# Kernel optimization log

Hardware: AMD Instinct MI355X
Metric: run time of the kernel (lower is better)

The kernel has to match this reference:

```python
import jax, jax.numpy as jnp
import numpy as np

HIDDEN = 2048
HEADS = 16
HEAD_DIM = HIDDEN // HEADS
TOP_K = 256
B, N = 1, 2048


def setup_inputs() -> dict:
    key = jax.random.key(0)
    ks = jax.random.split(key, 9)
    s = 0.02
    return {
        "hidden_states": jax.random.normal(ks[0], (B, N, HIDDEN), jnp.float32),
        "Wq": jax.random.normal(ks[1], (HIDDEN, HIDDEN), jnp.float32) * s,
        "bq": jnp.zeros((HIDDEN,), jnp.float32),
        "Wk": jax.random.normal(ks[2], (HIDDEN, HIDDEN), jnp.float32) * s,
        "bk": jnp.zeros((HIDDEN,), jnp.float32),
        "Wv": jax.random.normal(ks[3], (HIDDEN, HIDDEN), jnp.float32) * s,
        "bv": jnp.zeros((HIDDEN,), jnp.float32),
        "Wo": jax.random.normal(ks[4], (HIDDEN, HIDDEN), jnp.float32) * s,
        "bo": jnp.zeros((HIDDEN,), jnp.float32),
    }


def _split_heads(x):
    b, n, _ = x.shape
    return x.reshape(b, n, HEADS, HEAD_DIM).transpose(0, 2, 1, 3)  # b h n d


def reference(hidden_states, Wq, bq, Wk, bk, Wv, bv, Wo, bo):
    scale = 1.0 / jnp.sqrt(jnp.float32(HEAD_DIM))
    q = _split_heads(hidden_states @ Wq + bq)  # [b,h,n,d]
    k = _split_heads(hidden_states @ Wk + bk)
    v = _split_heads(hidden_states @ Wv + bv)

    # Sparse path (kv_seq_length > attention_window): dense QK^T used only to rank keys.
    scores = jnp.einsum("bhnd,bhmd->bhnm", q, k) * scale  # [b,h,n,n]
    importance = scores.mean(axis=2)  # [b,h,n] aggregate over queries
    _, idx = jax.lax.top_k(importance, TOP_K)  # [b,h,k]

    # gather selected K/V (torch.gather along seq dim)
    k_sel = jnp.take_along_axis(k, idx[..., None], axis=2)  # [b,h,k,d]
    v_sel = jnp.take_along_axis(v, idx[..., None], axis=2)

    w = jax.nn.softmax(jnp.einsum("bhnd,bhkd->bhnk", q, k_sel) * scale, axis=-1)
    out = jnp.einsum("bhnk,bhkd->bhnd", w, v_sel)  # [b,h,n,d]
    out = out.transpose(0, 2, 1, 3).reshape(hidden_states.shape[0], -1, HIDDEN)
    return out @ Wo + bo
```

## Files before the change

kernel.cpp:

```cpp
#include <hip/hip_runtime.h>


typedef __attribute__((ext_vector_type(8))) short bf16x8;
typedef __attribute__((ext_vector_type(8))) unsigned short u16x8;
typedef __attribute__((ext_vector_type(4))) float f32x4;

__device__ __forceinline__ unsigned short f2bf(float x) {
    unsigned u = __float_as_uint(x);
    u += 0x7fffu + ((u >> 16) & 1u);
    return (unsigned short)(u >> 16);
}

__device__ __forceinline__ void load_lds16(const unsigned short* g, unsigned short* l) {
    __builtin_amdgcn_global_load_lds(
        (const __attribute__((address_space(1))) unsigned int*)g,
        (__attribute__((address_space(3))) unsigned int*)l,
        16, 0, 0);
}

struct Ptr4  { const float* p[4]; };

__global__ __launch_bounds__(256) void gemm_qkv(
    const unsigned short* __restrict__ HSb,
    const unsigned short* __restrict__ WT4,
    const float* __restrict__ bq,
    const float* __restrict__ bk,
    const float* __restrict__ bv,
    const int* __restrict__ idx,
    unsigned short* __restrict__ Qb,
    unsigned short* __restrict__ Ksel,
    unsigned short* __restrict__ VselT)
{
    __shared__ __align__(16) unsigned short As[4][128][32];
    __shared__ __align__(16) unsigned short Bs[4][64][32];

    const int tid  = threadIdx.x;
    const int lane = tid & 63;
    const int wave = tid >> 6;
    const int wm = wave >> 1, wn = wave & 1;
    const int lr  = lane >> 2;
    const int scc = (((lane & 3) ^ ((lr >> 1) & 3))) * 8;
    const int rc  = (((lane >> 4) ^ (((lane & 15) >> 1) & 3))) * 8;

    const int bid = blockIdx.x;

    int kv, h = 0, bm, bn;
    const unsigned short* Bt;
    long ar0, ar1;
    if (bid < 128) {
        kv = 1 + (bid >> 6);
        const int t = bid & 63;
        h  = t >> 2;
        bm = ((t >> 1) & 1) * 128;
        bn = h * 128 + (t & 1) * 64;
        Bt = WT4 + (long)kv * 4194304;
        ar0 = idx[h * 256 + bm + wave * 16 + lr];
        ar1 = idx[h * 256 + bm + wave * 16 + 64 + lr];
    } else {
        kv = 0;
        const int t = bid - 128;
        const int tl = (t & 7) * 64 + (t >> 3);
        const int st = tl >> 5, u = tl & 31;
        bm = ((st >> 2) * 4 + (u >> 3)) * 128;
        bn = ((st & 3) * 8 + (u & 7)) * 64;
        Bt = WT4;
        ar0 = bm + wave * 16 + lr;
        ar1 = ar0 + 64;
    }

    const unsigned short* Arow0 = HSb + ar0 * 2048 + scc;
    const unsigned short* Arow1 = HSb + ar1 * 2048 + scc;
    const unsigned short* Brow0 = Bt + (long)(bn + wave * 16 + lr) * 2048 + scc;

    f32x4 acc[4][2];
#pragma unroll
    for (int i = 0; i < 4; i++)
#pragma unroll
        for (int j = 0; j < 2; j++) acc[i][j] = f32x4{0.f, 0.f, 0.f, 0.f};

    auto stage = [&](int b, int step) {
        const int k0 = step * 32;
        load_lds16(Arow0 + k0, &As[b][wave * 16][0]);
        load_lds16(Arow1 + k0, &As[b][wave * 16 + 64][0]);
        load_lds16(Brow0 + k0, &Bs[b][wave * 16][0]);
    };
    auto compute = [&](int b) {
        bf16x8 af[4], bf[2];
#pragma unroll
        for (int s = 0; s < 4; s++)
            af[s] = *(const bf16x8*)&As[b][wm * 64 + s * 16 + (lane & 15)][rc];
#pragma unroll
        for (int t = 0; t < 2; t++)
            bf[t] = *(const bf16x8*)&Bs[b][wn * 32 + t * 16 + (lane & 15)][rc];
#pragma unroll
        for (int s = 0; s < 4; s++)
#pragma unroll
            for (int t = 0; t < 2; t++)
                acc[s][t] = __builtin_amdgcn_mfma_f32_16x16x32_bf16(af[s], bf[t], acc[s][t], 0, 0, 0);
    };

    stage(0, 0);
    stage(1, 1);
    stage(2, 2);
#pragma unroll 4
    for (int t = 0; t < 61; ++t) {
        asm volatile("s_waitcnt vmcnt(6)" ::: "memory");
        __builtin_amdgcn_s_barrier();
        __builtin_amdgcn_sched_barrier(0);
        stage((t + 3) & 3, t + 3);
        __builtin_amdgcn_sched_barrier(0);
        compute(t & 3);
    }
    asm volatile("s_waitcnt vmcnt(6)" ::: "memory");
    __builtin_amdgcn_s_barrier();
    __builtin_amdgcn_sched_barrier(0);
    compute(1);
    asm volatile("s_waitcnt vmcnt(3)" ::: "memory");
    __builtin_amdgcn_s_barrier();
    __builtin_amdgcn_sched_barrier(0);
    compute(2);
    asm volatile("s_waitcnt vmcnt(0)" ::: "memory");
    __builtin_amdgcn_s_barrier();
    __builtin_amdgcn_sched_barrier(0);
    compute(3);

    if (kv == 0) {
#pragma unroll
        for (int s = 0; s < 4; s++) {
#pragma unroll
            for (int t = 0; t < 2; t++) {
                const int col  = bn + wn * 32 + t * 16 + (lane & 15);
                const int row0 = bm + wm * 64 + s * 16 + (lane >> 4) * 4;
                const float bb = bq[col];
#pragma unroll
                for (int r = 0; r < 4; r++)
                    Qb[(long)(row0 + r) * 2048 + col] = f2bf(acc[s][t][r] + bb);
            }
        }
    } else {
        const float* bp = (kv == 1) ? bk : bv;
#pragma unroll
        for (int s = 0; s < 4; s++) {
#pragma unroll
            for (int t = 0; t < 2; t++) {
                const int col = bn + wn * 32 + t * 16 + (lane & 15);
                const int dd  = col & 127;
                const float bb = bp[col];
                const int j0 = bm + wm * 64 + s * 16 + (lane >> 4) * 4;
#pragma unroll
                for (int r = 0; r < 4; r++) {
                    const int j = j0 + r;
                    const unsigned short h16 = f2bf(acc[s][t][r] + bb);
                    if (kv == 1) Ksel [h * 32768 + j * 128 + dd] = h16;
                    else         VselT[h * 32768 + dd * 256 + j] = h16;
                }
            }
        }
    }
}

__global__ __launch_bounds__(256) void gemm_o(
    const unsigned short* __restrict__ Att,
    const unsigned short* __restrict__ WoT,
    const float* __restrict__ bo,
    float* __restrict__ out)
{
    __shared__ __align__(16) unsigned short As[4][128][32];
    __shared__ __align__(16) unsigned short Bs[4][64][32];

    const int tid  = threadIdx.x;
    const int lane = tid & 63;
    const int wave = tid >> 6;
    const int wm = wave >> 1, wn = wave & 1;
    const int lr  = lane >> 2;
    const int scc = (((lane & 3) ^ ((lr >> 1) & 3))) * 8;
    const int rc  = (((lane >> 4) ^ (((lane & 15) >> 1) & 3))) * 8;

    const int t0 = blockIdx.x;
    const int tl = (t0 & 7) * 64 + (t0 >> 3);
    const int st = tl >> 5, u = tl & 31;
    const int bm = ((st >> 2) * 4 + (u >> 3)) * 128;
    const int bn = ((st & 3) * 8 + (u & 7)) * 64;

    const unsigned short* Arow0 = Att + (long)(bm + wave * 16 + lr) * 2048 + scc;
    const unsigned short* Arow1 = Arow0 + 64 * 2048;
    const unsigned short* Brow0 = WoT + (long)(bn + wave * 16 + lr) * 2048 + scc;

    f32x4 acc[4][2];
#pragma unroll
    for (int i = 0; i < 4; i++)
#pragma unroll
        for (int j = 0; j < 2; j++) acc[i][j] = f32x4{0.f, 0.f, 0.f, 0.f};

    auto stage = [&](int b, int step) {
        const int k0 = step * 32;
        load_lds16(Arow0 + k0, &As[b][wave * 16][0]);
        load_lds16(Arow1 + k0, &As[b][wave * 16 + 64][0]);
        load_lds16(Brow0 + k0, &Bs[b][wave * 16][0]);
    };
    auto compute = [&](int b) {
        bf16x8 af[4], bf[2];
#pragma unroll
        for (int s = 0; s < 4; s++)
            af[s] = *(const bf16x8*)&As[b][wm * 64 + s * 16 + (lane & 15)][rc];
#pragma unroll
        for (int t = 0; t < 2; t++)
            bf[t] = *(const bf16x8*)&Bs[b][wn * 32 + t * 16 + (lane & 15)][rc];
#pragma unroll
        for (int s = 0; s < 4; s++)
#pragma unroll
            for (int t = 0; t < 2; t++)
                acc[s][t] = __builtin_amdgcn_mfma_f32_16x16x32_bf16(af[s], bf[t], acc[s][t], 0, 0, 0);
    };

    stage(0, 0);
    stage(1, 1);
    stage(2, 2);
#pragma unroll 4
    for (int t = 0; t < 61; ++t) {
        asm volatile("s_waitcnt vmcnt(6)" ::: "memory");
        __builtin_amdgcn_s_barrier();
        __builtin_amdgcn_sched_barrier(0);
        stage((t + 3) & 3, t + 3);
        __builtin_amdgcn_sched_barrier(0);
        compute(t & 3);
    }
    asm volatile("s_waitcnt vmcnt(6)" ::: "memory");
    __builtin_amdgcn_s_barrier();
    __builtin_amdgcn_sched_barrier(0);
    compute(1);
    asm volatile("s_waitcnt vmcnt(3)" ::: "memory");
    __builtin_amdgcn_s_barrier();
    __builtin_amdgcn_sched_barrier(0);
    compute(2);
    asm volatile("s_waitcnt vmcnt(0)" ::: "memory");
    __builtin_amdgcn_s_barrier();
    __builtin_amdgcn_sched_barrier(0);
    compute(3);

#pragma unroll
    for (int s = 0; s < 4; s++) {
#pragma unroll
        for (int t = 0; t < 2; t++) {
            const int col  = bn + wn * 32 + t * 16 + (lane & 15);
            const int row0 = bm + wm * 64 + s * 16 + (lane >> 4) * 4;
            const float bb = bo[col];
#pragma unroll
            for (int r = 0; r < 4; r++)
                out[(long)(row0 + r) * 2048 + col] = acc[s][t][r] + bb;
        }
    }
}

#define QS_OFF(c)  ((c) * 2048)
#define KS_OFF(c)  (4096 + (c) * 8192)
#define PS_OFF     0
#define VS_OFF(c)  (16896 + (c) * 4096)

__global__ __launch_bounds__(256, 2) void attn_kernel(
    const unsigned short* __restrict__ Qb,
    const unsigned short* __restrict__ Ksel,
    const unsigned short* __restrict__ VselT,
    unsigned short* __restrict__ Att)
{
    __shared__ __align__(16) unsigned short smem[25088];
    __shared__ float linv[64];

    const int tid  = threadIdx.x;
    const int lane = tid & 63;
    const int wave = tid >> 6;
    const int bm = blockIdx.x * 64;
    const int h  = blockIdx.y;
    const int lr  = lane >> 2;
    const int scc = (((lane & 3) ^ ((lr >> 1) & 3))) * 8;
    const int rc  = (((lane >> 4) ^ (((lane & 15) >> 1) & 3))) * 8;

    const unsigned short* Kh = Ksel  + h * 32768;
    const unsigned short* Vh = VselT + h * 32768;

    f32x4 acc[16];
#pragma unroll
    for (int t = 0; t < 16; t++) acc[t] = f32x4{0.f, 0.f, 0.f, 0.f};

#pragma unroll
    for (int c2 = 0; c2 < 2; c2++) {
        __syncthreads();
#pragma unroll
        for (int c = 0; c < 2; c++) {
            const int k0 = c2 * 64 + c * 32;
            load_lds16(Qb + (long)(bm + wave * 16 + lr) * 2048 + h * 128 + k0 + scc,
                       &smem[QS_OFF(c) + wave * 512]);
#pragma unroll
            for (int q = 0; q < 4; q++)
                load_lds16(Kh + (wave * 64 + q * 16 + lr) * 128 + k0 + scc,
                           &smem[KS_OFF(c) + (wave * 64 + q * 16) * 32]);
        }
        __syncthreads();
#pragma unroll
        for (int kk = 0; kk < 2; kk++) {
            bf16x8 af = *(const bf16x8*)&smem[QS_OFF(kk) + (wave * 16 + (lane & 15)) * 32 + rc];
#pragma unroll
            for (int t = 0; t < 16; t++) {
                bf16x8 bfv = *(const bf16x8*)&smem[KS_OFF(kk) + (t * 16 + (lane & 15)) * 32 + rc];
                acc[t] = __builtin_amdgcn_mfma_f32_16x16x32_bf16(af, bfv, acc[t], 0, 0, 0);
            }
        }
    }
    __syncthreads();

    const float se = 0.08838834764831845f * 1.4426950408889634f;
#pragma unroll
    for (int r = 0; r < 4; r++) {
        float mx = -3.0e38f;
#pragma unroll
        for (int t = 0; t < 16; t++) mx = fmaxf(mx, acc[t][r]);
#pragma unroll
        for (int off = 1; off < 16; off <<= 1) mx = fmaxf(mx, __shfl_xor(mx, off));
        float sum = 0.f;
#pragma unroll
        for (int t = 0; t < 16; t++) {
            float p = exp2f((acc[t][r] - mx) * se);
            acc[t][r] = p;
            sum += p;
        }
#pragma unroll
        for (int off = 1; off < 16; off <<= 1) sum += __shfl_xor(sum, off);
        const int row = wave * 16 + (lane >> 4) * 4 + r;
#pragma unroll
        for (int t = 0; t < 16; t++)
            smem[PS_OFF + row * 264 + t * 16 + (lane & 15)] = f2bf(acc[t][r]);
        if ((lane & 15) == 0) linv[row] = 1.0f / sum;
    }

    const int wm2 = wave >> 1, wn2 = wave & 1;
    f32x4 acc2[2][4];
#pragma unroll
    for (int i = 0; i < 2; i++)
#pragma unroll
        for (int j = 0; j < 4; j++) acc2[i][j] = f32x4{0.f, 0.f, 0.f, 0.f};

#pragma unroll
    for (int c2 = 0; c2 < 4; c2++) {
#pragma unroll
        for (int c = 0; c < 2; c++) {
            const int j0 = c2 * 64 + c * 32;
#pragma unroll
            for (int q = 0; q < 2; q++)
                load_lds16(Vh + (wave * 32 + q * 16 + lr) * 256 + j0 + scc,
                           &smem[VS_OFF(c) + (wave * 32 + q * 16) * 32]);
        }
        __syncthreads();
#pragma unroll
        for (int c = 0; c < 2; c++) {
            const int j0 = c2 * 64 + c * 32;
            bf16x8 af2[2], bf2v[4];
#pragma unroll
            for (int s2 = 0; s2 < 2; s2++)
                af2[s2] = *(const bf16x8*)&smem[PS_OFF + (wm2 * 32 + s2 * 16 + (lane & 15)) * 264 + j0 + (lane >> 4) * 8];
#pragma unroll
            for (int t2 = 0; t2 < 4; t2++)
                bf2v[t2] = *(const bf16x8*)&smem[VS_OFF(c) + (wn2 * 64 + t2 * 16 + (lane & 15)) * 32 + rc];
#pragma unroll
            for (int s2 = 0; s2 < 2; s2++)
#pragma unroll
                for (int t2 = 0; t2 < 4; t2++)
                    acc2[s2][t2] = __builtin_amdgcn_mfma_f32_16x16x32_bf16(af2[s2], bf2v[t2], acc2[s2][t2], 0, 0, 0);
        }
        __syncthreads();
    }

#pragma unroll
    for (int s2 = 0; s2 < 2; s2++) {
#pragma unroll
        for (int t2 = 0; t2 < 4; t2++) {
            const int d = wn2 * 64 + t2 * 16 + (lane & 15);
#pragma unroll
            for (int r = 0; r < 4; r++) {
                const int row = wm2 * 32 + s2 * 16 + (lane >> 4) * 4 + r;
                float v = acc2[s2][t2][r] * linv[row];
                Att[(long)(bm + row) * 2048 + h * 128 + d] = f2bf(v);
            }
        }
    }
}

__global__ __launch_bounds__(256) void prep_kernel(Ptr4 srcs, unsigned short* __restrict__ WT4,
                                                   const float* __restrict__ hs,
                                                   double* __restrict__ part) {
    const int b = blockIdx.x;
    const int tid = threadIdx.x;
    if (b < 4096) {
        __shared__ float tile[64][65];
        const int z = b >> 10, xy = b & 1023;
        const float* W = srcs.p[z];
        unsigned short* WT = WT4 + (long)z * 4194304;
        const int bx = (xy & 31) * 64;
        const int by = (xy >> 5) * 64;
        const int x = tid & 63, y = tid >> 6;
#pragma unroll
        for (int i = 0; i < 64; i += 4)
            tile[y + i][x] = W[(long)(by + y + i) * 2048 + bx + x];
        __syncthreads();
#pragma unroll
        for (int i = 0; i < 64; i += 4)
            WT[(long)(bx + y + i) * 2048 + by + x] = f2bf(tile[x][y + i]);
    } else {
        const int c = b - 4096;
        const int col = (c & 7) * 256 + tid;
        const int r0  = (c >> 3) * 32;
        double a = 0.0;
#pragma unroll 4
        for (int r = 0; r < 32; r++) a += (double)hs[(long)(r0 + r) * 2048 + col];
        part[(long)(c >> 3) * 2048 + col] = a;
    }
}

__global__ void fill_kernel(float* p, float v, long n) {
    long i = ((long)blockIdx.x * blockDim.x + threadIdx.x) * 4;
    if (i + 3 < n) { p[i] = v; p[i+1] = v; p[i+2] = v; p[i+3] = v; }
}

__global__ __launch_bounds__(256) void mean_qsum_part(const double* __restrict__ part,
                                                      const float* __restrict__ Wq,
                                                      double* __restrict__ partq) {
    __shared__ float hsb[32];
    const int j  = blockIdx.x * 256 + threadIdx.x;
    const int i0 = blockIdx.y * 32;
    if (threadIdx.x < 32) {
        double s = 0.0;
#pragma unroll 4
        for (int g = 0; g < 64; g++) s += part[(long)g * 2048 + i0 + threadIdx.x];
        hsb[threadIdx.x] = (float)(s * (1.0 / 2048.0));
    }
    __syncthreads();
    double a = 0.0;
#pragma unroll 4
    for (int r = 0; r < 32; r++)
        a += (double)hsb[r] * (double)Wq[(long)(i0 + r) * 2048 + j];
    partq[(long)blockIdx.y * 2048 + j] = a;
}

__global__ void qsum_fin(const double* __restrict__ partq, const float* __restrict__ bq,
                         float* __restrict__ qbar) {
    const int j = blockIdx.x * 64 + threadIdx.x;
    double s = (double)bq[j];
#pragma unroll 4
    for (int g = 0; g < 64; g++) s += partq[(long)g * 2048 + j];
    qbar[j] = (float)s;
}

__global__ __launch_bounds__(256) void u_kernel(const float* __restrict__ Wk,
                                                const float* __restrict__ qbar,
                                                float* __restrict__ U) {
    const int i = blockIdx.x, t = threadIdx.x;
#pragma unroll
    for (int r = 0; r < 2; r++) {
        const int e = r * 1024 + t * 4;
        float4 w = *(const float4*)(Wk + (long)i * 2048 + e);
        float4 q = *(const float4*)(qbar + e);
        float a = w.x * q.x + w.y * q.y + w.z * q.z + w.w * q.w;
#pragma unroll
        for (int off = 16; off; off >>= 1) a += __shfl_xor(a, off);
        if ((t & 31) == 0) U[(long)i * 16 + r * 8 + (t >> 5)] = a;
    }
}

__global__ __launch_bounds__(256) void cast_imp_kernel(const float* __restrict__ hs,
                                                       const float* __restrict__ U,
                                                       unsigned short* __restrict__ HSb,
                                                       float* __restrict__ imp) {
    __shared__ float red[4][4][16];
    const int m0 = blockIdx.x * 4, t = threadIdx.x;

    float va[4][8];
#pragma unroll
    for (int r = 0; r < 4; r++) {
        const float4 v0 = *(const float4*)(hs + (long)(m0 + r) * 2048 + t * 8);
        const float4 v1 = *(const float4*)(hs + (long)(m0 + r) * 2048 + t * 8 + 4);
        va[r][0] = v0.x; va[r][1] = v0.y; va[r][2] = v0.z; va[r][3] = v0.w;
        va[r][4] = v1.x; va[r][5] = v1.y; va[r][6] = v1.z; va[r][7] = v1.w;
        u16x8 hb;
#pragma unroll
        for (int j = 0; j < 8; j++) hb[j] = f2bf(va[r][j]);
        *(u16x8*)(HSb + (long)(m0 + r) * 2048 + t * 8) = hb;
    }

    float p[4][16];
#pragma unroll
    for (int r = 0; r < 4; r++)
#pragma unroll
        for (int h = 0; h < 16; h++) p[r][h] = 0.f;

    const float4* Uq = (const float4*)(U + (long)t * 128);
#pragma unroll
    for (int j = 0; j < 8; j++) {
        const float4 u0 = Uq[j * 4 + 0];
        const float4 u1 = Uq[j * 4 + 1];
        const float4 u2 = Uq[j * 4 + 2];
        const float4 u3 = Uq[j * 4 + 3];
#pragma unroll
        for (int r = 0; r < 4; r++) {
            const float v = va[r][j];
            p[r][0]  += v * u0.x; p[r][1]  += v * u0.y; p[r][2]  += v * u0.z; p[r][3]  += v * u0.w;
            p[r][4]  += v * u1.x; p[r][5]  += v * u1.y; p[r][6]  += v * u1.z; p[r][7]  += v * u1.w;
            p[r][8]  += v * u2.x; p[r][9]  += v * u2.y; p[r][10] += v * u2.z; p[r][11] += v * u2.w;
            p[r][12] += v * u3.x; p[r][13] += v * u3.y; p[r][14] += v * u3.z; p[r][15] += v * u3.w;
        }
    }

#pragma unroll
    for (int off = 32; off; off >>= 1)
#pragma unroll
        for (int r = 0; r < 4; r++)
#pragma unroll
            for (int h = 0; h < 16; h++) p[r][h] += __shfl_down(p[r][h], off);
    if ((t & 63) == 0)
#pragma unroll
        for (int r = 0; r < 4; r++)
#pragma unroll
            for (int h = 0; h < 16; h++) red[t >> 6][r][h] = p[r][h];
    __syncthreads();
    if (t < 64) {
        const int h = t & 15, r = t >> 4;
        imp[(long)h * 2048 + m0 + r] =
            red[0][r][h] + red[1][r][h] + red[2][r][h] + red[3][r][h];
    }
}

__global__ __launch_bounds__(64) void topk_idx(const float* __restrict__ imp,
                                               int* __restrict__ idx) {
    const int h = blockIdx.x;
    const int lane = threadIdx.x;
    unsigned u[32];
#pragma unroll
    for (int r = 0; r < 32; r++) {
        unsigned x = __float_as_uint(imp[(long)h * 2048 + r * 64 + lane]);
        u[r] = (x & 0x80000000u) ? ~x : (x | 0x80000000u);
    }
    unsigned cur = 0;
    for (int b = 31; b >= 0; b--) {
        const unsigned cand = cur | (1u << b);
        int tot = 0;
#pragma unroll
        for (int r = 0; r < 32; r++)
            tot += (int)__popcll(__ballot(u[r] >= cand));
        if (tot >= 256) cur = cand;
    }
    const unsigned long long below = (1ull << lane) - 1ull;
    int pos[32];
    int base = 0;
#pragma unroll
    for (int r = 0; r < 32; r++) {
        const bool q = u[r] > cur;
        const unsigned long long m = __ballot(q);
        pos[r] = q ? base + (int)__popcll(m & below) : -1;
        base += (int)__popcll(m);
    }
#pragma unroll
    for (int r = 0; r < 32; r++) {
        const bool q = (u[r] == cur);
        const unsigned long long m = __ballot(q);
        if (q) {
            const int p = base + (int)__popcll(m & below);
            pos[r] = (p < 256) ? p : -1;
        }
        base += (int)__popcll(m);
    }
#pragma unroll
    for (int r = 0; r < 32; r++)
        if (pos[r] >= 0) idx[h * 256 + pos[r]] = r * 64 + lane;
}

extern "C" void kernel_launch(void* const* d_in, const int* in_sizes, int n_in,
                              void* d_out, int out_size, void* d_ws, size_t ws_size,
                              hipStream_t stream)
{
    const float* hs = (const float*)d_in[0];
    const float* Wq = (const float*)d_in[1];
    const float* bq = (const float*)d_in[2];
    const float* Wk = (const float*)d_in[3];
    const float* bk = (const float*)d_in[4];
    const float* Wv = (const float*)d_in[5];
    const float* bv = (const float*)d_in[6];
    const float* Wo = (const float*)d_in[7];
    const float* bo = (const float*)d_in[8];

    char* ws = (char*)d_ws;
    size_t off = 0;
    auto alloc = [&](size_t b) -> void* {
        void* p = ws + off;
        off = (off + b + 255) & ~(size_t)255;
        return p;
    };
    unsigned short* HSb   = (unsigned short*)alloc(8388608);
    unsigned short* WT4   = (unsigned short*)alloc(4 * 8388608);
    unsigned short* Qb    = (unsigned short*)alloc(8388608);
    unsigned short* Att   = (unsigned short*)alloc(8388608);
    unsigned short* Ksel  = (unsigned short*)alloc(1048576);
    unsigned short* VselT = (unsigned short*)alloc(1048576);
    double* part  = (double*)alloc(1048576);
    double* partq = (double*)alloc(1048576);
    float* qbar  = (float*)alloc(8192);
    float* U     = (float*)alloc(131072);
    float* imp   = (float*)alloc(131072);
    int*   idx   = (int*)alloc(16384);

    if (off > ws_size) {
        fill_kernel<<<4096, 256, 0, stream>>>((float*)d_out, 12345.0f, (long)out_size);
        return;
    }

    unsigned short* WoT = WT4 + 3 * 4194304;

    prep_kernel<<<4608, 256, 0, stream>>>(Ptr4{{Wq, Wk, Wv, Wo}}, WT4, hs, part);

    mean_qsum_part<<<dim3(8, 64), 256, 0, stream>>>(part, Wq, partq);
    qsum_fin<<<32, 64, 0, stream>>>(partq, bq, qbar);
    u_kernel<<<2048, 256, 0, stream>>>(Wk, qbar, U);
    cast_imp_kernel<<<512, 256, 0, stream>>>(hs, U, HSb, imp);

    topk_idx<<<16, 64, 0, stream>>>(imp, idx);

    gemm_qkv<<<640, 256, 0, stream>>>(HSb, WT4, bq, bk, bv, idx, Qb, Ksel, VselT);

    attn_kernel<<<dim3(32, 16), 256, 0, stream>>>(Qb, Ksel, VselT, Att);

    gemm_o<<<512, 256, 0, stream>>>(Att, WoT, bo, (float*)d_out);
}
```

Before: 279.5 us.

## Deepen QKV GEMM pipeline to six LDS buffers processed in pairs

Grows the QKV projection GEMM's LDS ring from 4 to 6 stages. Each barrier now issues two k-steps of global-to-LDS loads and computes two k-steps, which halves the number of barriers per tile. The same change drops the XOR swizzle of the LDS column layout and the tile-index remap for the Q blocks, going back to plain row-major staging and linear block order. In exchange it uses more LDS per block, which can lower occupancy, and risks LDS bank conflicts and worse L2 locality.

```diff
diff --git a/kernel.cpp b/kernel.cpp
--- a/kernel.cpp
+++ b/kernel.cpp
@@ -31,16 +31,15 @@
     unsigned short* __restrict__ Ksel,
     unsigned short* __restrict__ VselT)
 {
-    __shared__ __align__(16) unsigned short As[4][128][32];
-    __shared__ __align__(16) unsigned short Bs[4][64][32];
+    __shared__ __align__(16) unsigned short As[6][128][32];
+    __shared__ __align__(16) unsigned short Bs[6][64][32];
 
     const int tid  = threadIdx.x;
     const int lane = tid & 63;
     const int wave = tid >> 6;
     const int wm = wave >> 1, wn = wave & 1;
-    const int lr  = lane >> 2;
-    const int scc = (((lane & 3) ^ ((lr >> 1) & 3))) * 8;
-    const int rc  = (((lane >> 4) ^ (((lane & 15) >> 1) & 3))) * 8;
+    const int lr = lane >> 2;
+    const int lc = (lane & 3) * 8;
 
     const int bid = blockIdx.x;
 
@@ -59,8 +58,7 @@
     } else {
         kv = 0;
         const int t = bid - 128;
-        const int tl = (t & 7) * 64 + (t >> 3);
-        const int st = tl >> 5, u = tl & 31;
+        const int st = t >> 5, u = t & 31;
         bm = ((st >> 2) * 4 + (u >> 3)) * 128;
         bn = ((st & 3) * 8 + (u & 7)) * 64;
         Bt = WT4;
@@ -68,9 +66,9 @@
         ar1 = ar0 + 64;
     }
 
-    const unsigned short* Arow0 = HSb + ar0 * 2048 + scc;
-    const unsigned short* Arow1 = HSb + ar1 * 2048 + scc;
-    const unsigned short* Brow0 = Bt + (long)(bn + wave * 16 + lr) * 2048 + scc;
+    const unsigned short* Arow0 = HSb + ar0 * 2048 + lc;
+    const unsigned short* Arow1 = HSb + ar1 * 2048 + lc;
+    const unsigned short* Brow0 = Bt + (long)(bn + wave * 16 + lr) * 2048 + lc;
 
     f32x4 acc[4][2];
 #pragma unroll
@@ -88,41 +86,42 @@
         bf16x8 af[4], bf[2];
 #pragma unroll
         for (int s = 0; s < 4; s++)
-            af[s] = *(const bf16x8*)&As[b][wm * 64 + s * 16 + (lane & 15)][rc];
+            af[s] = *(const bf16x8*)&As[b][wm * 64 + s * 16 + (lane & 15)][(lane >> 4) * 8];
 #pragma unroll
         for (int t = 0; t < 2; t++)
-            bf[t] = *(const bf16x8*)&Bs[b][wn * 32 + t * 16 + (lane & 15)][rc];
+            bf[t] = *(const bf16x8*)&Bs[b][wn * 32 + t * 16 + (lane & 15)][(lane >> 4) * 8];
 #pragma unroll
         for (int s = 0; s < 4; s++)
 #pragma unroll
             for (int t = 0; t < 2; t++)
                 acc[s][t] = __builtin_amdgcn_mfma_f32_16x16x32_bf16(af[s], bf[t], acc[s][t], 0, 0, 0);
     };
-
-    stage(0, 0);
-    stage(1, 1);
-    stage(2, 2);
-#pragma unroll 4
-    for (int t = 0; t < 61; ++t) {
+    auto pairstep = [&](int ca, int cb, int sa, int sb, int stepA) {
         asm volatile("s_waitcnt vmcnt(6)" ::: "memory");
         __builtin_amdgcn_s_barrier();
         __builtin_amdgcn_sched_barrier(0);
-        stage((t + 3) & 3, t + 3);
+        stage(sa, stepA);
+        stage(sb, stepA + 1);
         __builtin_amdgcn_sched_barrier(0);
-        compute(t & 3);
+        compute(ca);
+        compute(cb);
+    };
+
+    stage(0, 0); stage(1, 1); stage(2, 2); stage(3, 3);
+    for (int g = 0; g < 10; ++g) {
+        const int b6 = g * 6;
+        pairstep(0, 1, 4, 5, b6 + 4);
+        pairstep(2, 3, 0, 1, b6 + 6);
+        pairstep(4, 5, 2, 3, b6 + 8);
     }
     asm volatile("s_waitcnt vmcnt(6)" ::: "memory");
     __builtin_amdgcn_s_barrier();
     __builtin_amdgcn_sched_barrier(0);
-    compute(1);
-    asm volatile("s_waitcnt vmcnt(3)" ::: "memory");
-    __builtin_amdgcn_s_barrier();
-    __builtin_amdgcn_sched_barrier(0);
-    compute(2);
+    compute(0); compute(1);
     asm volatile("s_waitcnt vmcnt(0)" ::: "memory");
     __builtin_amdgcn_s_barrier();
     __builtin_amdgcn_sched_barrier(0);
-    compute(3);
+    compute(2); compute(3);
 
     if (kv == 0) {
 #pragma unroll
```

New measurement: 285.4 us. +2.1%, slower.
